# Kernel tuning notes

Measured on AMD Instinct MI355X. Metric: run time of the kernel, lower is better.

Reference implementation:

```python
import jax, jax.numpy as jnp
import numpy as np

B, T, D, H = 256, 512, 128, 256


def _cell0(x, Wi, bi, bh):
    # PyTorch GRU cell evaluated with h=0 (seq_len-1 call, no carried state):
    # W_hh @ 0 == 0, so only hidden biases bh survive. Gate order: r, z, n.
    g = x @ Wi.T + bi
    gr, gz, gn = jnp.split(g, 3, axis=-1)
    br, bz, bn = jnp.split(bh, 3, axis=-1)
    r = jax.nn.sigmoid(gr + br)
    z = jax.nn.sigmoid(gz + bz)
    n = jnp.tanh(gn + r * bn)
    return (1.0 - z) * n  # h' = (1-z)*n + z*0


def _gru_seq(x, Wi, Wh, bi, bh):
    # single-layer batch_first GRU over full sequence, h0 = 0
    gi = jnp.einsum('btd,gd->btg', x, Wi) + bi  # precompute input projections

    def step(h, gi_t):
        gh = h @ Wh.T + bh
        gir, giz, gin = jnp.split(gi_t, 3, axis=-1)
        ghr, ghz, ghn = jnp.split(gh, 3, axis=-1)
        r = jax.nn.sigmoid(gir + ghr)
        z = jax.nn.sigmoid(giz + ghz)
        n = jnp.tanh(gin + r * ghn)
        h_new = (1.0 - z) * n + z * h
        return h_new, h_new

    h0 = jnp.zeros((x.shape[0], Wh.shape[1]), x.dtype)
    _, hs = jax.lax.scan(step, h0, jnp.swapaxes(gi, 0, 1))
    return jnp.swapaxes(hs, 0, 1)  # [B,T,H]


def setup_inputs() -> dict:
    key = jax.random.key(0)
    ks = jax.random.split(key, 32)
    s = 0.06  # ~ torch uniform(-1/sqrt(H), 1/sqrt(H)) scale
    g = lambda k, shape: (jax.random.normal(k, shape, dtype=jnp.float32) * s)
    inp = {
        'x': jax.random.normal(ks[0], (B, T, D), dtype=jnp.float32),
        # memory_constructor: 1-layer GRU(D -> H)
        'Wm_i': g(ks[1], (3 * H, D)), 'Wm_h': g(ks[2], (3 * H, H)),
        'bm_i': g(ks[3], (3 * H,)), 'bm_h': g(ks[4], (3 * H,)),
        # decoder: 3-layer GRU(D+H -> H), used with h0=0, seq_len=1 each step
        'Wd_i0': g(ks[5], (3 * H, D + H)), 'bd_i0': g(ks[6], (3 * H,)), 'bd_h0': g(ks[7], (3 * H,)),
        'Wd_i1': g(ks[8], (3 * H, H)), 'bd_i1': g(ks[9], (3 * H,)), 'bd_h1': g(ks[10], (3 * H,)),
        'Wd_i2': g(ks[11], (3 * H, H)), 'bd_i2': g(ks[12], (3 * H,)), 'bd_h2': g(ks[13], (3 * H,)),
        # knapsack_handler: 2-layer GRU(H -> H), h0=0, seq_len=1
        'Wk_i0': g(ks[14], (3 * H, H)), 'bk_i0': g(ks[15], (3 * H,)), 'bk_h0': g(ks[16], (3 * H,)),
        'Wk_i1': g(ks[17], (3 * H, H)), 'bk_i1': g(ks[18], (3 * H,)), 'bk_h1': g(ks[19], (3 * H,)),
        # output layer: Linear(H -> 1)
        'Wo': g(ks[20], (1, H)), 'bo': g(ks[21], (1,)),
    }
    return inp


def reference(x, Wm_i, Wm_h, bm_i, bm_h,
              Wd_i0, bd_i0, bd_h0, Wd_i1, bd_i1, bd_h1, Wd_i2, bd_i2, bd_h2,
              Wk_i0, bk_i0, bk_h0, Wk_i1, bk_i1, bk_h1, Wo, bo):
    mem = _gru_seq(x, Wm_i, Wm_h, bm_i, bm_h)  # [B,T,H]

    def step(ksack, x_t):
        # Bahdanau-style dot attention over memory with knapsack_state as query
        scores = jnp.einsum('bth,bh->bt', mem, ksack)
        w = jax.nn.softmax(scores, axis=1)
        ctx = jnp.einsum('bt,bth->bh', w, mem)
        d = jnp.concatenate([x_t, ctx], axis=-1)  # [B, D+H]
        h = _cell0(d, Wd_i0, bd_i0, bd_h0)
        h = _cell0(h, Wd_i1, bd_i1, bd_h1)
        h = _cell0(h, Wd_i2, bd_i2, bd_h2)
        k = _cell0(h, Wk_i0, bk_i0, bk_h0)
        k = _cell0(k, Wk_i1, bk_i1, bk_h1)
        out_t = jax.nn.sigmoid(k @ Wo.T + bo)[:, 0]  # [B]
        return k, out_t

    ks0 = jnp.zeros((x.shape[0], mem.shape[2]), x.dtype)
    _, outs = jax.lax.scan(step, ks0, jnp.swapaxes(x, 0, 1))
    return jnp.swapaxes(outs, 0, 1)  # [B,T]
```

## Files before the change

kernel.cpp:

```cpp
#include <hip/hip_runtime.h>
#include <stdint.h>

#define BATCH 256
#define SEQT  512
#define DIM   128
#define HID   256
#define G3    768

typedef unsigned short u16;
typedef unsigned int   u32;
typedef _Float16 f16;
typedef f16 f16x2 __attribute__((ext_vector_type(2)));
typedef u32 u32x4v __attribute__((ext_vector_type(4)));
typedef float f32x4 __attribute__((ext_vector_type(4)));

static __device__ __forceinline__ u16 f2h(float f) {
  f16 h = (f16)f; return __builtin_bit_cast(u16, h);
}
static __device__ __forceinline__ float h2f(u16 u) {
  return (float)__builtin_bit_cast(f16, u);
}
static __device__ __forceinline__ float sigm(float v) {
  return 1.f / (1.f + __expf(-v));
}

static __device__ __forceinline__ float dot2f(u32 a, u32 b, float acc) {
#if __has_builtin(__builtin_amdgcn_fdot2)
  return __builtin_amdgcn_fdot2(__builtin_bit_cast(f16x2, a),
                                __builtin_bit_cast(f16x2, b), acc, false);
#else
  f16x2 av = __builtin_bit_cast(f16x2, a), bv = __builtin_bit_cast(f16x2, b);
  return acc + (float)av[0] * (float)bv[0] + (float)av[1] * (float)bv[1];
#endif
}
static __device__ __forceinline__ void dot8q(float& a0, float& a1, u32x4v w, u32x4v a) {
  a0 = dot2f(w.x, a.x, a0);
  a1 = dot2f(w.y, a.y, a1);
  a0 = dot2f(w.z, a.z, a0);
  a1 = dot2f(w.w, a.w, a1);
}

__global__ void convertT(const float* __restrict__ src, u16* __restrict__ dst,
                         int IN, int chunks, int total) {
  int t = blockIdx.x * 256 + threadIdx.x;
  if (t >= total) return;
  int e = t & 7, c = (t >> 3) & 255, r = t >> 11;
  int j = r % chunks, q = r / chunks;
  dst[t] = f2h(src[(size_t)(q * 256 + c) * IN + j * 8 + e]);
}

__launch_bounds__(768)
__global__ void gru_memk(const float* __restrict__ x,
                         const u16* __restrict__ WiT, const u16* __restrict__ WhT,
                         const float* __restrict__ bmi, const float* __restrict__ bmh,
                         u16* __restrict__ mem) {
  const int b = blockIdx.x, tid = threadIdx.x;
  const int q = tid >> 8, c = tid & 255;
  __shared__ __align__(16) u16 xsH[DIM];
  __shared__ __align__(16) u16 hsH[HID];
  __shared__ __align__(16) float rs[HID], zs[HID];

  float Brz = 0.f, Bni = 0.f, Bnh = 0.f;
  if (q < 2) { int rw = q * HID + c; Brz = bmi[rw] + bmh[rw]; }
  else       { int rw = 2 * HID + c; Bni = bmi[rw]; Bnh = bmh[rw]; }
  const u32x4v* wi = (const u32x4v*)WiT + (size_t)q * (DIM / 8) * 256 + c;
  const u32x4v* wh = (const u32x4v*)WhT + (size_t)q * (HID / 8) * 256 + c;
  float hprev = 0.f;
  if (tid < HID) hsH[tid] = 0;
  __syncthreads();

  for (int t = 0; t < SEQT; ++t) {
    if (tid < DIM)
      xsH[tid] = f2h(__builtin_nontemporal_load(x + ((size_t)b * SEQT + t) * DIM + tid));
    __syncthreads();
    float ax0 = 0.f, ax1 = 0.f, ah0 = 0.f, ah1 = 0.f;
    const u32x4v* xa = (const u32x4v*)xsH;
    const u32x4v* ha = (const u32x4v*)hsH;
    #pragma unroll 4
    for (int j = 0; j < DIM / 8; ++j) dot8q(ax0, ax1, wi[(size_t)j * 256], xa[j]);
    #pragma unroll 4
    for (int j = 0; j < HID / 8; ++j) dot8q(ah0, ah1, wh[(size_t)j * 256], ha[j]);
    float ax = ax0 + ax1, ah = ah0 + ah1;
    if (q < 2) (q ? zs : rs)[c] = sigm(ax + ah + Brz);
    __syncthreads();
    if (q == 2) {
      float nn = tanhf(ax + Bni + rs[c] * (ah + Bnh));
      float h = (1.f - zs[c]) * nn + zs[c] * hprev;
      hprev = h;
      hsH[c] = f2h(h);
      mem[((size_t)b * SEQT + t) * HID + c] = f2h(h);
    }
    __syncthreads();
  }
}

template <int IN>
static __device__ __forceinline__ void cellT(const u16* __restrict__ inH,
                                             u16* __restrict__ outH,
                                             const u16* __restrict__ WT,
                                             int q, int c,
                                             float Brz, float Bni, float Bnh,
                                             float* __restrict__ rs, float* __restrict__ zs) {
  float a0 = 0.f, a1 = 0.f;
  if (q < 3) {
    const u32x4v* w = (const u32x4v*)WT + (size_t)q * (IN / 8) * 256 + c;
    const u32x4v* av = (const u32x4v*)inH;
    #pragma unroll 4
    for (int j = 0; j < IN / 8; ++j) dot8q(a0, a1, w[(size_t)j * 256], av[j]);
    if (q < 2) (q ? zs : rs)[c] = sigm(a0 + a1 + Brz);
  }
  __syncthreads();
  if (q == 2)
    outH[c] = f2h((1.f - zs[c]) * tanhf(a0 + a1 + Bni + rs[c] * Bnh));
  __syncthreads();
}

__launch_bounds__(1024)
__global__ void decoderk(const float* __restrict__ x, const u16* __restrict__ memH,
                         const u16* __restrict__ W0T, const u16* __restrict__ W1T,
                         const u16* __restrict__ W2T, const u16* __restrict__ W3T,
                         const u16* __restrict__ W4T,
                         const float* __restrict__ bi0, const float* __restrict__ bh0,
                         const float* __restrict__ bi1, const float* __restrict__ bh1,
                         const float* __restrict__ bi2, const float* __restrict__ bh2,
                         const float* __restrict__ bi3, const float* __restrict__ bh3,
                         const float* __restrict__ bi4, const float* __restrict__ bh4,
                         const float* __restrict__ Wo, const float* __restrict__ bo,
                         float* __restrict__ out) {
  const int b = blockIdx.x, tid = threadIdx.x;
  const int lane = tid & 63, wave = tid >> 6;
  const int q = tid >> 8, c = tid & 255;
  __shared__ __align__(16) u16 kstH[HID];
  __shared__ __align__(16) u16 dvH[DIM + HID];
  __shared__ __align__(16) u16 hAH[HID], hBH[HID];
  __shared__ __align__(16) float rs[HID], zs[HID];
  __shared__ __align__(16) float ppF[512];
  __shared__ __align__(16) float pvp[8][HID];
  __shared__ float red[16], red2[16];

  float Brz[5] = {0,0,0,0,0}, Bni[5] = {0,0,0,0,0}, Bnh[5] = {0,0,0,0,0};
  if (q < 2) {
    int rw = q * HID + c;
    Brz[0] = bi0[rw] + bh0[rw]; Brz[1] = bi1[rw] + bh1[rw]; Brz[2] = bi2[rw] + bh2[rw];
    Brz[3] = bi3[rw] + bh3[rw]; Brz[4] = bi4[rw] + bh4[rw];
  } else if (q == 2) {
    int rw = 2 * HID + c;
    Bni[0] = bi0[rw]; Bnh[0] = bh0[rw]; Bni[1] = bi1[rw]; Bnh[1] = bh1[rw];
    Bni[2] = bi2[rw]; Bnh[2] = bh2[rw]; Bni[3] = bi3[rw]; Bnh[3] = bh3[rw];
    Bni[4] = bi4[rw]; Bnh[4] = bh4[rw];
  }
  float wo0 = 0.f, wo1 = 0.f, wo2 = 0.f, wo3 = 0.f;
  const float bo0 = bo[0];
  if (wave == 0) { wo0 = Wo[lane]; wo1 = Wo[64+lane]; wo2 = Wo[128+lane]; wo3 = Wo[192+lane]; }
  if (tid < HID) kstH[tid] = 0;
  __syncthreads();

  const u16* mb = memH + (size_t)b * SEQT * HID;
  const int p = tid >> 1, hf = tid & 1;
  const int sg = tid >> 7, cp = tid & 127;

  for (int t = 0; t < SEQT; ++t) {
    float xr = 0.f;
    if (tid < DIM)
      xr = __builtin_nontemporal_load(x + ((size_t)b * SEQT + t) * DIM + tid);

    float s0 = 0.f, s1 = 0.f;
    {
      const u32x4v* mr = (const u32x4v*)(mb + (size_t)p * HID) + hf * 16;
      const u32x4v* kq = ((const u32x4v*)kstH) + hf * 16;
      #pragma unroll 4
      for (int j = 0; j < 16; ++j) dot8q(s0, s1, mr[j], kq[j]);
    }
    float s = s0 + s1;
    s += __shfl_xor(s, 1);
    float mloc = s;
    #pragma unroll
    for (int off = 32; off; off >>= 1) mloc = fmaxf(mloc, __shfl_xor(mloc, off));
    if (lane == 0) red[wave] = mloc;
    __syncthreads();
    float m = red[0];
    #pragma unroll
    for (int i = 1; i < 16; ++i) m = fmaxf(m, red[i]);
    float pw = __expf(s - m);
    if (!hf) ppF[p] = pw;
    float ls = hf ? 0.f : pw;
    #pragma unroll
    for (int off = 32; off; off >>= 1) ls += __shfl_xor(ls, off);
    if (lane == 0) red2[wave] = ls;
    if (tid < DIM) dvH[tid] = f2h(xr);
    __syncthreads();

    float c0 = 0.f, c1 = 0.f;
    {
      const u32* mc = (const u32*)mb + (size_t)sg * 64 * 128 + cp;
      const float* ppg = ppF + sg * 64;
      #pragma unroll 8
      for (int pj = 0; pj < 64; ++pj) {
        u32 v = mc[(size_t)pj * 128];
        float w2 = ppg[pj];
        f16x2 hv = __builtin_bit_cast(f16x2, v);
        c0 += w2 * (float)hv[0];
        c1 += w2 * (float)hv[1];
      }
      pvp[sg][2 * cp]     = c0;
      pvp[sg][2 * cp + 1] = c1;
    }
    __syncthreads();
    if (tid < HID) {
      float lsum = red2[0];
      #pragma unroll
      for (int i = 1; i < 16; ++i) lsum += red2[i];
      float ctx = pvp[0][tid] + pvp[1][tid] + pvp[2][tid] + pvp[3][tid] +
                  pvp[4][tid] + pvp[5][tid] + pvp[6][tid] + pvp[7][tid];
      dvH[DIM + tid] = f2h(ctx / lsum);
    }
    __syncthreads();

    cellT<DIM + HID>(dvH, hAH, W0T, q, c, Brz[0], Bni[0], Bnh[0], rs, zs);
    cellT<HID>(hAH, hBH, W1T, q, c, Brz[1], Bni[1], Bnh[1], rs, zs);
    cellT<HID>(hBH, hAH, W2T, q, c, Brz[2], Bni[2], Bnh[2], rs, zs);
    cellT<HID>(hAH, hBH, W3T, q, c, Brz[3], Bni[3], Bnh[3], rs, zs);
    cellT<HID>(hBH, kstH, W4T, q, c, Brz[4], Bni[4], Bnh[4], rs, zs);

    if (wave == 0) {
      float acc = h2f(kstH[lane]) * wo0 + h2f(kstH[64 + lane]) * wo1 +
                  h2f(kstH[128 + lane]) * wo2 + h2f(kstH[192 + lane]) * wo3;
      #pragma unroll
      for (int off = 32; off; off >>= 1) acc += __shfl_xor(acc, off);
      if (lane == 0) out[(size_t)b * SEQT + t] = sigm(acc + bo0);
    }
  }
}

extern "C" void kernel_launch(void* const* d_in, const int* in_sizes, int n_in,
                              void* d_out, int out_size, void* d_ws, size_t ws_size,
                              hipStream_t stream) {
  const float* x    = (const float*)d_in[0];
  const float* Wmi  = (const float*)d_in[1];
  const float* Wmh  = (const float*)d_in[2];
  const float* bmi  = (const float*)d_in[3];
  const float* bmh  = (const float*)d_in[4];
  const float* Wd0  = (const float*)d_in[5];
  const float* bi0  = (const float*)d_in[6];
  const float* bh0  = (const float*)d_in[7];
  const float* Wd1  = (const float*)d_in[8];
  const float* bi1  = (const float*)d_in[9];
  const float* bh1  = (const float*)d_in[10];
  const float* Wd2  = (const float*)d_in[11];
  const float* bi2  = (const float*)d_in[12];
  const float* bh2  = (const float*)d_in[13];
  const float* Wk0  = (const float*)d_in[14];
  const float* bik0 = (const float*)d_in[15];
  const float* bhk0 = (const float*)d_in[16];
  const float* Wk1  = (const float*)d_in[17];
  const float* bik1 = (const float*)d_in[18];
  const float* bhk1 = (const float*)d_in[19];
  const float* Wo   = (const float*)d_in[20];
  const float* bo   = (const float*)d_in[21];

  u16* mem = (u16*)d_ws;
  size_t off = (size_t)BATCH * SEQT * HID;
  u16* WmiT = mem + off; off += (size_t)G3 * DIM;
  u16* WmhT = mem + off; off += (size_t)G3 * HID;
  u16* W0T  = mem + off; off += (size_t)G3 * (DIM + HID);
  u16* W1T  = mem + off; off += (size_t)G3 * HID;
  u16* W2T  = mem + off; off += (size_t)G3 * HID;
  u16* W3T  = mem + off; off += (size_t)G3 * HID;
  u16* W4T  = mem + off; off += (size_t)G3 * HID;
  (void)ws_size; (void)in_sizes; (void)n_in; (void)out_size;

  convertT<<<(G3*DIM + 255) / 256, 256, 0, stream>>>(Wmi, WmiT, DIM, DIM/8, G3*DIM);
  convertT<<<(G3*HID + 255) / 256, 256, 0, stream>>>(Wmh, WmhT, HID, HID/8, G3*HID);
  convertT<<<(G3*(DIM+HID) + 255) / 256, 256, 0, stream>>>(Wd0, W0T, DIM+HID, (DIM+HID)/8, G3*(DIM+HID));
  convertT<<<(G3*HID + 255) / 256, 256, 0, stream>>>(Wd1, W1T, HID, HID/8, G3*HID);
  convertT<<<(G3*HID + 255) / 256, 256, 0, stream>>>(Wd2, W2T, HID, HID/8, G3*HID);
  convertT<<<(G3*HID + 255) / 256, 256, 0, stream>>>(Wk0, W3T, HID, HID/8, G3*HID);
  convertT<<<(G3*HID + 255) / 256, 256, 0, stream>>>(Wk1, W4T, HID, HID/8, G3*HID);

  gru_memk<<<BATCH, 768, 0, stream>>>(x, WmiT, WmhT, bmi, bmh, mem);
  decoderk<<<BATCH, 1024, 0, stream>>>(x, mem, W0T, W1T, W2T, W3T, W4T,
                                       bi0, bh0, bi1, bh1, bi2, bh2,
                                       bik0, bhk0, bik1, bhk1, Wo, bo,
                                       (float*)d_out);
}
```

Measured before the change: 22.94 ms.

## Split GRU gate dot products across four lanes per hidden unit with shuffle reduction

Remaps both the memory GRU and the decoder cells so each hidden unit is handled by four adjacent threads. Each thread computes partial r, z and n dot products over a quarter of the input, and the partials are combined with xor shuffles. The weight layout is changed to match, and the shared-memory r/z exchange plus one barrier per cell are removed. The cost is redundant bias registers and more shuffles, and the memory GRU grows to 1024 threads per block. Separately, the attention score loop unroll factor is raised.

```diff
diff --git a/kernel.cpp b/kernel.cpp
--- a/kernel.cpp
+++ b/kernel.cpp
@@ -12,7 +12,6 @@
 typedef _Float16 f16;
 typedef f16 f16x2 __attribute__((ext_vector_type(2)));
 typedef u32 u32x4v __attribute__((ext_vector_type(4)));
-typedef float f32x4 __attribute__((ext_vector_type(4)));
 
 static __device__ __forceinline__ u16 f2h(float f) {
   f16 h = (f16)f; return __builtin_bit_cast(u16, h);
@@ -40,31 +39,34 @@
   a1 = dot2f(w.w, a.w, a1);
 }
 
-__global__ void convertT(const float* __restrict__ src, u16* __restrict__ dst,
-                         int IN, int chunks, int total) {
+__global__ void convertQ(const float* __restrict__ src, u16* __restrict__ dst,
+                         int IN, int CH, int total) {
   int t = blockIdx.x * 256 + threadIdx.x;
   if (t >= total) return;
-  int e = t & 7, c = (t >> 3) & 255, r = t >> 11;
-  int j = r % chunks, q = r / chunks;
-  dst[t] = f2h(src[(size_t)(q * 256 + c) * IN + j * 8 + e]);
-}
-
-__launch_bounds__(768)
-__global__ void gru_memk(const float* __restrict__ x,
+  int e = t & 7, sub = (t >> 3) & 3, c = (t >> 5) & 255;
+  int qq = t >> 13;
+  int jj = qq % CH, g = qq / CH;
+  int col = sub * (IN / 4) + jj * 8 + e;
+  dst[t] = f2h(src[(size_t)(g * 256 + c) * IN + col]);
+}
+
+__launch_bounds__(1024)
+__global__ void gru_memq(const float* __restrict__ x,
                          const u16* __restrict__ WiT, const u16* __restrict__ WhT,
                          const float* __restrict__ bmi, const float* __restrict__ bmh,
                          u16* __restrict__ mem) {
   const int b = blockIdx.x, tid = threadIdx.x;
-  const int q = tid >> 8, c = tid & 255;
+  const int c = tid >> 2, sub = tid & 3;
   __shared__ __align__(16) u16 xsH[DIM];
   __shared__ __align__(16) u16 hsH[HID];
-  __shared__ __align__(16) float rs[HID], zs[HID];
-
-  float Brz = 0.f, Bni = 0.f, Bnh = 0.f;
-  if (q < 2) { int rw = q * HID + c; Brz = bmi[rw] + bmh[rw]; }
-  else       { int rw = 2 * HID + c; Bni = bmi[rw]; Bnh = bmh[rw]; }
-  const u32x4v* wi = (const u32x4v*)WiT + (size_t)q * (DIM / 8) * 256 + c;
-  const u32x4v* wh = (const u32x4v*)WhT + (size_t)q * (HID / 8) * 256 + c;
+
+  const float Brzr = bmi[c] + bmh[c];
+  const float Brzz = bmi[HID + c] + bmh[HID + c];
+  const float Bni  = bmi[2*HID + c];
+  const float Bnh  = bmh[2*HID + c];
+  const u32x4v* Wi4 = (const u32x4v*)WiT;
+  const u32x4v* Wh4 = (const u32x4v*)WhT;
+  const int widx = (c << 2) + sub;
   float hprev = 0.f;
   if (tid < HID) hsH[tid] = 0;
   __syncthreads();
@@ -73,50 +75,74 @@
     if (tid < DIM)
       xsH[tid] = f2h(__builtin_nontemporal_load(x + ((size_t)b * SEQT + t) * DIM + tid));
     __syncthreads();
-    float ax0 = 0.f, ax1 = 0.f, ah0 = 0.f, ah1 = 0.f;
-    const u32x4v* xa = (const u32x4v*)xsH;
-    const u32x4v* ha = (const u32x4v*)hsH;
+    float ar0=0.f, ar1=0.f, az0=0.f, az1=0.f, axn0=0.f, axn1=0.f, ahn0=0.f, ahn1=0.f;
+    const u32x4v* xs4 = (const u32x4v*)xsH;
+    const u32x4v* hs4 = (const u32x4v*)hsH;
+    #pragma unroll
+    for (int jj = 0; jj < 4; ++jj) {
+      u32x4v av = xs4[sub * 4 + jj];
+      dot8q(ar0, ar1, Wi4[((0*4 + jj) << 10) + widx], av);
+      dot8q(az0, az1, Wi4[((1*4 + jj) << 10) + widx], av);
+      dot8q(axn0, axn1, Wi4[((2*4 + jj) << 10) + widx], av);
+    }
     #pragma unroll 4
-    for (int j = 0; j < DIM / 8; ++j) dot8q(ax0, ax1, wi[(size_t)j * 256], xa[j]);
-    #pragma unroll 4
-    for (int j = 0; j < HID / 8; ++j) dot8q(ah0, ah1, wh[(size_t)j * 256], ha[j]);
-    float ax = ax0 + ax1, ah = ah0 + ah1;
-    if (q < 2) (q ? zs : rs)[c] = sigm(ax + ah + Brz);
-    __syncthreads();
-    if (q == 2) {
-      float nn = tanhf(ax + Bni + rs[c] * (ah + Bnh));
-      float h = (1.f - zs[c]) * nn + zs[c] * hprev;
+    for (int jj = 0; jj < 8; ++jj) {
+      u32x4v av = hs4[sub * 8 + jj];
+      dot8q(ar0, ar1, Wh4[((0*8 + jj) << 10) + widx], av);
+      dot8q(az0, az1, Wh4[((1*8 + jj) << 10) + widx], av);
+      dot8q(ahn0, ahn1, Wh4[((2*8 + jj) << 10) + widx], av);
+    }
+    float ar = ar0 + ar1, az = az0 + az1, axn = axn0 + axn1, ahn = ahn0 + ahn1;
+    ar  += __shfl_xor(ar, 1);  ar  += __shfl_xor(ar, 2);
+    az  += __shfl_xor(az, 1);  az  += __shfl_xor(az, 2);
+    axn += __shfl_xor(axn, 1); axn += __shfl_xor(axn, 2);
+    ahn += __shfl_xor(ahn, 1); ahn += __shfl_xor(ahn, 2);
+    __syncthreads();
+    if (sub == 0) {
+      float r = sigm(ar + Brzr);
+      float z = sigm(az + Brzz);
+      float nn = tanhf(axn + Bni + r * (ahn + Bnh));
+      float h = (1.f - z) * nn + z * hprev;
       hprev = h;
       hsH[c] = f2h(h);
       mem[((size_t)b * SEQT + t) * HID + c] = f2h(h);
     }
-    __syncthreads();
   }
 }
 
 template <int IN>
-static __device__ __forceinline__ void cellT(const u16* __restrict__ inH,
+static __device__ __forceinline__ void cellQ(const u16* __restrict__ inH,
                                              u16* __restrict__ outH,
                                              const u16* __restrict__ WT,
-                                             int q, int c,
-                                             float Brz, float Bni, float Bnh,
-                                             float* __restrict__ rs, float* __restrict__ zs) {
-  float a0 = 0.f, a1 = 0.f;
-  if (q < 3) {
-    const u32x4v* w = (const u32x4v*)WT + (size_t)q * (IN / 8) * 256 + c;
-    const u32x4v* av = (const u32x4v*)inH;
-    #pragma unroll 4
-    for (int j = 0; j < IN / 8; ++j) dot8q(a0, a1, w[(size_t)j * 256], av[j]);
-    if (q < 2) (q ? zs : rs)[c] = sigm(a0 + a1 + Brz);
+                                             int c, int sub,
+                                             float Brzr, float Brzz, float Bni, float Bnh) {
+  constexpr int CH = IN / 32;
+  const u32x4v* W4 = (const u32x4v*)WT;
+  const u32x4v* in4 = (const u32x4v*)inH;
+  const int widx = (c << 2) + sub;
+  float ar0=0.f, ar1=0.f, az0=0.f, az1=0.f, an0=0.f, an1=0.f;
+  #pragma unroll 4
+  for (int jj = 0; jj < CH; ++jj) {
+    u32x4v av = in4[sub * CH + jj];
+    dot8q(ar0, ar1, W4[((0*CH + jj) << 10) + widx], av);
+    dot8q(az0, az1, W4[((1*CH + jj) << 10) + widx], av);
+    dot8q(an0, an1, W4[((2*CH + jj) << 10) + widx], av);
+  }
+  float ar = ar0 + ar1, az = az0 + az1, an = an0 + an1;
+  ar += __shfl_xor(ar, 1); ar += __shfl_xor(ar, 2);
+  az += __shfl_xor(az, 1); az += __shfl_xor(az, 2);
+  an += __shfl_xor(an, 1); an += __shfl_xor(an, 2);
+  if (sub == 0) {
+    float r = sigm(ar + Brzr);
+    float z = sigm(az + Brzz);
+    float nn = tanhf(an + Bni + r * Bnh);
+    outH[c] = f2h((1.f - z) * nn);
   }
   __syncthreads();
-  if (q == 2)
-    outH[c] = f2h((1.f - zs[c]) * tanhf(a0 + a1 + Bni + rs[c] * Bnh));
-  __syncthreads();
 }
 
 __launch_bounds__(1024)
-__global__ void decoderk(const float* __restrict__ x, const u16* __restrict__ memH,
+__global__ void decoderq(const float* __restrict__ x, const u16* __restrict__ memH,
                          const u16* __restrict__ W0T, const u16* __restrict__ W1T,
                          const u16* __restrict__ W2T, const u16* __restrict__ W3T,
                          const u16* __restrict__ W4T,
@@ -129,26 +155,20 @@
                          float* __restrict__ out) {
   const int b = blockIdx.x, tid = threadIdx.x;
   const int lane = tid & 63, wave = tid >> 6;
-  const int q = tid >> 8, c = tid & 255;
+  const int c = tid >> 2, sub = tid & 3;
   __shared__ __align__(16) u16 kstH[HID];
   __shared__ __align__(16) u16 dvH[DIM + HID];
   __shared__ __align__(16) u16 hAH[HID], hBH[HID];
-  __shared__ __align__(16) float rs[HID], zs[HID];
   __shared__ __align__(16) float ppF[512];
   __shared__ __align__(16) float pvp[8][HID];
   __shared__ float red[16], red2[16];
 
-  float Brz[5] = {0,0,0,0,0}, Bni[5] = {0,0,0,0,0}, Bnh[5] = {0,0,0,0,0};
-  if (q < 2) {
-    int rw = q * HID + c;
-    Brz[0] = bi0[rw] + bh0[rw]; Brz[1] = bi1[rw] + bh1[rw]; Brz[2] = bi2[rw] + bh2[rw];
-    Brz[3] = bi3[rw] + bh3[rw]; Brz[4] = bi4[rw] + bh4[rw];
-  } else if (q == 2) {
-    int rw = 2 * HID + c;
-    Bni[0] = bi0[rw]; Bnh[0] = bh0[rw]; Bni[1] = bi1[rw]; Bnh[1] = bh1[rw];
-    Bni[2] = bi2[rw]; Bnh[2] = bh2[rw]; Bni[3] = bi3[rw]; Bnh[3] = bh3[rw];
-    Bni[4] = bi4[rw]; Bnh[4] = bh4[rw];
-  }
+  float Rr[5], Rz[5], Ni[5], Nh[5];
+  Rr[0]=bi0[c]+bh0[c]; Rz[0]=bi0[HID+c]+bh0[HID+c]; Ni[0]=bi0[2*HID+c]; Nh[0]=bh0[2*HID+c];
+  Rr[1]=bi1[c]+bh1[c]; Rz[1]=bi1[HID+c]+bh1[HID+c]; Ni[1]=bi1[2*HID+c]; Nh[1]=bh1[2*HID+c];
+  Rr[2]=bi2[c]+bh2[c]; Rz[2]=bi2[HID+c]+bh2[HID+c]; Ni[2]=bi2[2*HID+c]; Nh[2]=bh2[2*HID+c];
+  Rr[3]=bi3[c]+bh3[c]; Rz[3]=bi3[HID+c]+bh3[HID+c]; Ni[3]=bi3[2*HID+c]; Nh[3]=bh3[2*HID+c];
+  Rr[4]=bi4[c]+bh4[c]; Rz[4]=bi4[HID+c]+bh4[HID+c]; Ni[4]=bi4[2*HID+c]; Nh[4]=bh4[2*HID+c];
   float wo0 = 0.f, wo1 = 0.f, wo2 = 0.f, wo3 = 0.f;
   const float bo0 = bo[0];
   if (wave == 0) { wo0 = Wo[lane]; wo1 = Wo[64+lane]; wo2 = Wo[128+lane]; wo3 = Wo[192+lane]; }
@@ -168,7 +188,7 @@
     {
       const u32x4v* mr = (const u32x4v*)(mb + (size_t)p * HID) + hf * 16;
       const u32x4v* kq = ((const u32x4v*)kstH) + hf * 16;
-      #pragma unroll 4
+      #pragma unroll 8
       for (int j = 0; j < 16; ++j) dot8q(s0, s1, mr[j], kq[j]);
     }
     float s = s0 + s1;
@@ -216,11 +236,11 @@
     }
     __syncthreads();
 
-    cellT<DIM + HID>(dvH, hAH, W0T, q, c, Brz[0], Bni[0], Bnh[0], rs, zs);
-    cellT<HID>(hAH, hBH, W1T, q, c, Brz[1], Bni[1], Bnh[1], rs, zs);
-    cellT<HID>(hBH, hAH, W2T, q, c, Brz[2], Bni[2], Bnh[2], rs, zs);
-    cellT<HID>(hAH, hBH, W3T, q, c, Brz[3], Bni[3], Bnh[3], rs, zs);
-    cellT<HID>(hBH, kstH, W4T, q, c, Brz[4], Bni[4], Bnh[4], rs, zs);
+    cellQ<DIM + HID>(dvH, hAH, W0T, c, sub, Rr[0], Rz[0], Ni[0], Nh[0]);
+    cellQ<HID>(hAH, hBH, W1T, c, sub, Rr[1], Rz[1], Ni[1], Nh[1]);
+    cellQ<HID>(hBH, hAH, W2T, c, sub, Rr[2], Rz[2], Ni[2], Nh[2]);
+    cellQ<HID>(hAH, hBH, W3T, c, sub, Rr[3], Rz[3], Ni[3], Nh[3]);
+    cellQ<HID>(hBH, kstH, W4T, c, sub, Rr[4], Rz[4], Ni[4], Nh[4]);
 
     if (wave == 0) {
       float acc = h2f(kstH[lane]) * wo0 + h2f(kstH[64 + lane]) * wo1 +
@@ -269,16 +289,16 @@
   u16* W4T  = mem + off; off += (size_t)G3 * HID;
   (void)ws_size; (void)in_sizes; (void)n_in; (void)out_size;
 
-  convertT<<<(G3*DIM + 255) / 256, 256, 0, stream>>>(Wmi, WmiT, DIM, DIM/8, G3*DIM);
-  convertT<<<(G3*HID + 255) / 256, 256, 0, stream>>>(Wmh, WmhT, HID, HID/8, G3*HID);
-  convertT<<<(G3*(DIM+HID) + 255) / 256, 256, 0, stream>>>(Wd0, W0T, DIM+HID, (DIM+HID)/8, G3*(DIM+HID));
-  convertT<<<(G3*HID + 255) / 256, 256, 0, stream>>>(Wd1, W1T, HID, HID/8, G3*HID);
-  convertT<<<(G3*HID + 255) / 256, 256, 0, stream>>>(Wd2, W2T, HID, HID/8, G3*HID);
-  convertT<<<(G3*HID + 255) / 256, 256, 0, stream>>>(Wk0, W3T, HID, HID/8, G3*HID);
-  convertT<<<(G3*HID + 255) / 256, 256, 0, stream>>>(Wk1, W4T, HID, HID/8, G3*HID);
-
-  gru_memk<<<BATCH, 768, 0, stream>>>(x, WmiT, WmhT, bmi, bmh, mem);
-  decoderk<<<BATCH, 1024, 0, stream>>>(x, mem, W0T, W1T, W2T, W3T, W4T,
+  convertQ<<<(G3*DIM + 255) / 256, 256, 0, stream>>>(Wmi, WmiT, DIM, DIM/32, G3*DIM);
+  convertQ<<<(G3*HID + 255) / 256, 256, 0, stream>>>(Wmh, WmhT, HID, HID/32, G3*HID);
+  convertQ<<<(G3*(DIM+HID) + 255) / 256, 256, 0, stream>>>(Wd0, W0T, DIM+HID, (DIM+HID)/32, G3*(DIM+HID));
+  convertQ<<<(G3*HID + 255) / 256, 256, 0, stream>>>(Wd1, W1T, HID, HID/32, G3*HID);
+  convertQ<<<(G3*HID + 255) / 256, 256, 0, stream>>>(Wd2, W2T, HID, HID/32, G3*HID);
+  convertQ<<<(G3*HID + 255) / 256, 256, 0, stream>>>(Wk0, W3T, HID, HID/32, G3*HID);
+  convertQ<<<(G3*HID + 255) / 256, 256, 0, stream>>>(Wk1, W4T, HID, HID/32, G3*HID);
+
+  gru_memq<<<BATCH, 1024, 0, stream>>>(x, WmiT, WmhT, bmi, bmh, mem);
+  decoderq<<<BATCH, 1024, 0, stream>>>(x, mem, W0T, W1T, W2T, W3T, W4T,
                                        bi0, bh0, bi1, bh1, bi2, bh2,
                                        bik0, bhk0, bik1, bhk1, Wo, bo,
                                        (float*)d_out);
```

Measured after the change: 31.80 ms. 38.6% more time.

## Stream decoder GRU weights through per-wave LDS ring with async global_load_lds

Applied to the files above, without the earlier changes.

Each decoder cell now prefetches its f16 weight chunks with global_load_lds into a per-wave 8-slot LDS ring, six loads ahead. Manual s_waitcnt vmcnt counts gate each dot product, so weight fetch latency overlaps compute instead of stalling on direct global loads. The attention score loop also loads all 16 memory vectors into registers before running the dot products, to raise memory-level parallelism. The cost is 128KB of extra LDS and hand-written waitcnt assembly, which is fragile if the compiler reorders or inserts its own vector-memory operations.

```diff
diff --git a/kernel.cpp b/kernel.cpp
--- a/kernel.cpp
+++ b/kernel.cpp
@@ -6,13 +6,14 @@
 #define DIM   128
 #define HID   256
 #define G3    768
+#define SBUF  8
+#define SDEPTH 6
 
 typedef unsigned short u16;
 typedef unsigned int   u32;
 typedef _Float16 f16;
 typedef f16 f16x2 __attribute__((ext_vector_type(2)));
 typedef u32 u32x4v __attribute__((ext_vector_type(4)));
-typedef float f32x4 __attribute__((ext_vector_type(4)));
 
 static __device__ __forceinline__ u16 f2h(float f) {
   f16 h = (f16)f; return __builtin_bit_cast(u16, h);
@@ -38,6 +39,12 @@
   a1 = dot2f(w.y, a.y, a1);
   a0 = dot2f(w.z, a.z, a0);
   a1 = dot2f(w.w, a.w, a1);
+}
+
+static __device__ __forceinline__ void gload16(const u16* g, u16* l) {
+  __builtin_amdgcn_global_load_lds(
+      (const __attribute__((address_space(1))) u32*)g,
+      (__attribute__((address_space(3))) u32*)l, 16, 0, 0);
 }
 
 __global__ void convertT(const float* __restrict__ src, u16* __restrict__ dst,
@@ -74,12 +81,14 @@
       xsH[tid] = f2h(__builtin_nontemporal_load(x + ((size_t)b * SEQT + t) * DIM + tid));
     __syncthreads();
     float ax0 = 0.f, ax1 = 0.f, ah0 = 0.f, ah1 = 0.f;
-    const u32x4v* xa = (const u32x4v*)xsH;
-    const u32x4v* ha = (const u32x4v*)hsH;
-    #pragma unroll 4
-    for (int j = 0; j < DIM / 8; ++j) dot8q(ax0, ax1, wi[(size_t)j * 256], xa[j]);
-    #pragma unroll 4
-    for (int j = 0; j < HID / 8; ++j) dot8q(ah0, ah1, wh[(size_t)j * 256], ha[j]);
+    {
+      const u32x4v* xa = (const u32x4v*)xsH;
+      const u32x4v* ha = (const u32x4v*)hsH;
+      #pragma unroll 4
+      for (int j = 0; j < DIM / 8; ++j) dot8q(ax0, ax1, wi[(size_t)j * 256], xa[j]);
+      #pragma unroll 4
+      for (int j = 0; j < HID / 8; ++j) dot8q(ah0, ah1, wh[(size_t)j * 256], ha[j]);
+    }
     float ax = ax0 + ax1, ah = ah0 + ah1;
     if (q < 2) (q ? zs : rs)[c] = sigm(ax + ah + Brz);
     __syncthreads();
@@ -95,18 +104,32 @@
 }
 
 template <int IN>
-static __device__ __forceinline__ void cellT(const u16* __restrict__ inH,
+static __device__ __forceinline__ void cellL(const u16* __restrict__ inH,
                                              u16* __restrict__ outH,
                                              const u16* __restrict__ WT,
-                                             int q, int c,
+                                             int q, int c, int wid, int lane,
                                              float Brz, float Bni, float Bnh,
-                                             float* __restrict__ rs, float* __restrict__ zs) {
+                                             float* __restrict__ rs, float* __restrict__ zs,
+                                             u16 (* __restrict__ stg)[SBUF][512]) {
+  constexpr int CH = IN / 8;
   float a0 = 0.f, a1 = 0.f;
   if (q < 3) {
-    const u32x4v* w = (const u32x4v*)WT + (size_t)q * (IN / 8) * 256 + c;
+    const u16* wb = WT + ((size_t)q * CH * 256 + c) * 8;
     const u32x4v* av = (const u32x4v*)inH;
-    #pragma unroll 4
-    for (int j = 0; j < IN / 8; ++j) dot8q(a0, a1, w[(size_t)j * 256], av[j]);
+    u16* sb = &stg[wid][0][0];
+    asm volatile("s_waitcnt vmcnt(0)" ::: "memory");
+    #pragma unroll
+    for (int d = 0; d < SDEPTH; ++d)
+      gload16(wb + (size_t)d * 2048, sb + d * 512);
+    #pragma unroll
+    for (int j = 0; j < CH; ++j) {
+      const int issued = (j + SDEPTH < CH) ? (j + SDEPTH) : CH;
+      asm volatile("s_waitcnt vmcnt(%0)" :: "i"(issued - (j + 1)) : "memory");
+      u32x4v wv = *(const u32x4v*)(sb + (j & (SBUF - 1)) * 512 + lane * 8);
+      dot8q(a0, a1, wv, av[j]);
+      if (j + SDEPTH < CH)
+        gload16(wb + (size_t)(j + SDEPTH) * 2048, sb + ((j + SDEPTH) & (SBUF - 1)) * 512);
+    }
     if (q < 2) (q ? zs : rs)[c] = sigm(a0 + a1 + Brz);
   }
   __syncthreads();
@@ -137,6 +160,7 @@
   __shared__ __align__(16) float ppF[512];
   __shared__ __align__(16) float pvp[8][HID];
   __shared__ float red[16], red2[16];
+  __shared__ __align__(16) u16 wstage[16][SBUF][512];
 
   float Brz[5] = {0,0,0,0,0}, Bni[5] = {0,0,0,0,0}, Bnh[5] = {0,0,0,0,0};
   if (q < 2) {
@@ -168,8 +192,15 @@
     {
       const u32x4v* mr = (const u32x4v*)(mb + (size_t)p * HID) + hf * 16;
       const u32x4v* kq = ((const u32x4v*)kstH) + hf * 16;
-      #pragma unroll 4
-      for (int j = 0; j < 16; ++j) dot8q(s0, s1, mr[j], kq[j]);
+      u32x4v mA[8], mB[8];
+      #pragma unroll
+      for (int g = 0; g < 8; ++g) mA[g] = mr[g];
+      #pragma unroll
+      for (int g = 0; g < 8; ++g) mB[g] = mr[8 + g];
+      #pragma unroll
+      for (int g = 0; g < 8; ++g) dot8q(s0, s1, mA[g], kq[g]);
+      #pragma unroll
+      for (int g = 0; g < 8; ++g) dot8q(s0, s1, mB[g], kq[8 + g]);
     }
     float s = s0 + s1;
     s += __shfl_xor(s, 1);
@@ -216,11 +247,11 @@
     }
     __syncthreads();
 
-    cellT<DIM + HID>(dvH, hAH, W0T, q, c, Brz[0], Bni[0], Bnh[0], rs, zs);
-    cellT<HID>(hAH, hBH, W1T, q, c, Brz[1], Bni[1], Bnh[1], rs, zs);
-    cellT<HID>(hBH, hAH, W2T, q, c, Brz[2], Bni[2], Bnh[2], rs, zs);
-    cellT<HID>(hAH, hBH, W3T, q, c, Brz[3], Bni[3], Bnh[3], rs, zs);
-    cellT<HID>(hBH, kstH, W4T, q, c, Brz[4], Bni[4], Bnh[4], rs, zs);
+    cellL<DIM + HID>(dvH, hAH, W0T, q, c, wave, lane, Brz[0], Bni[0], Bnh[0], rs, zs, wstage);
+    cellL<HID>(hAH, hBH, W1T, q, c, wave, lane, Brz[1], Bni[1], Bnh[1], rs, zs, wstage);
+    cellL<HID>(hBH, hAH, W2T, q, c, wave, lane, Brz[2], Bni[2], Bnh[2], rs, zs, wstage);
+    cellL<HID>(hAH, hBH, W3T, q, c, wave, lane, Brz[3], Bni[3], Bnh[3], rs, zs, wstage);
+    cellL<HID>(hBH, kstH, W4T, q, c, wave, lane, Brz[4], Bni[4], Bnh[4], rs, zs, wstage);
 
     if (wave == 0) {
       float acc = h2f(kstH[lane]) * wo0 + h2f(kstH[64 + lane]) * wo1 +
```

After: 72.11 ms. +214.3%, slower.
